# Performance work log

Hardware: AMD Instinct MI355X
Metric: run time of the kernel (lower is better)

The kernel has to match this reference:

```python
import jax, jax.numpy as jnp
import numpy as np

MIN_NORM = 1e-15
C = 1.0  # ball curvature from init kwargs
N, D, O = 16384, 512, 512


def _expmap0(u, c):
    sqrt_c = c ** 0.5
    u_norm = jnp.maximum(jnp.linalg.norm(u, axis=-1, keepdims=True), MIN_NORM)
    return jnp.tanh(sqrt_c * u_norm) * u / (sqrt_c * u_norm)


def setup_inputs() -> dict:
    key = jax.random.key(0)
    k1, k2, k3 = jax.random.split(key, 3)
    # scale inputs so they lie inside the unit Poincare ball (E||x|| ~ 0.45)
    x = jax.random.normal(k1, (N, D), jnp.float32) * 0.02
    point = _expmap0(jax.random.normal(k2, (O, D), jnp.float32) / 4, C)
    tangent = jax.random.normal(k3, (O, D), jnp.float32)
    tangent = tangent / jnp.maximum(jnp.linalg.norm(tangent, axis=-1, keepdims=True), MIN_NORM)  # sphere proj_
    scale = jnp.zeros((O,), jnp.float32)
    return {"x": x, "point": point, "tangent": tangent, "scale": scale}


def reference(x, point, tangent, scale):
    """Mobius dist2plane (signed) * exp(scale).

    Computes the reductions of diff = mobius_add(-p, x) analytically so the
    [N, O, D] broadcast intermediate of the original is never materialized.
    """
    c = C
    sqrt_c = c ** 0.5
    p, a = point, tangent
    p2 = jnp.sum(p * p, -1)                 # [O]  ||p||^2
    x2 = jnp.sum(x * x, -1)                 # [N]  ||x||^2
    xp = x @ p.T                             # [N,O] <x, p>
    xy = -xp                                 # <-p, x>
    # mobius_add(-p, x) = (A*(-p) + B*x) / Dn
    A = 1 + 2 * c * xy + c * x2[:, None]     # [N,O] coeff of -p
    B = 1 - c * p2                           # [O]   coeff of x
    Dn = jnp.maximum(1 + 2 * c * xy + (c * c) * p2[None, :] * x2[:, None], MIN_NORM)  # [N,O]
    pa = jnp.sum(p * a, -1)                  # [O]  <p, a>
    xa = x @ a.T                             # [N,O] <x, a>
    diff_norm2 = (A * A * p2[None, :] - 2 * A * B[None, :] * xp
                  + (B * B)[None, :] * x2[:, None]) / (Dn * Dn)
    diff_norm2 = jnp.maximum(diff_norm2, MIN_NORM)
    sc_diff_a = (-A * pa[None, :] + B[None, :] * xa) / Dn  # <diff, a>
    a_norm = jnp.maximum(jnp.linalg.norm(a, axis=-1), MIN_NORM)  # [O]
    num = 2 * sqrt_c * sc_diff_a
    denom = jnp.maximum((1 - c * diff_norm2) * a_norm[None, :], MIN_NORM)
    dist = jnp.arcsinh(num / denom) / sqrt_c  # [N,O]
    return dist * jnp.exp(scale)
```

## Files before the change

kernel.cpp:

```cpp
#include <hip/hip_runtime.h>
#include <hip/hip_bf16.h>

typedef float f32x4 __attribute__((ext_vector_type(4)));
typedef short short8_t __attribute__((ext_vector_type(8)));

__device__ __forceinline__ unsigned int cvt2(float lo, float hi) {
    unsigned int ul = __builtin_bit_cast(unsigned int, lo);
    unsigned int uh = __builtin_bit_cast(unsigned int, hi);
    ul += 0x7FFFu + ((ul >> 16) & 1u);
    uh += 0x7FFFu + ((uh >> 16) & 1u);
    return (ul >> 16) | (uh & 0xFFFF0000u);
}

__device__ __forceinline__ float sq4(f32x4 v, float acc) {
    acc = fmaf(v[0], v[0], acc); acc = fmaf(v[1], v[1], acc);
    acc = fmaf(v[2], v[2], acc); acc = fmaf(v[3], v[3], acc);
    return acc;
}

__device__ __forceinline__ float dot4(f32x4 a, f32x4 b, float acc) {
    acc = fmaf(a[0], b[0], acc); acc = fmaf(a[1], b[1], acc);
    acc = fmaf(a[2], b[2], acc); acc = fmaf(a[3], b[3], acc);
    return acc;
}

__device__ __forceinline__ short8_t pk8(f32x4 a, f32x4 b) {
    union { short8_t s; unsigned int u[4]; } w;
    w.u[0] = cvt2(a[0], a[1]); w.u[1] = cvt2(a[2], a[3]);
    w.u[2] = cvt2(b[0], b[1]); w.u[3] = cvt2(b[2], b[3]);
    return w.s;
}

__device__ __forceinline__ void gload16(const void* g, void* l) {
    __builtin_amdgcn_global_load_lds(
        (const __attribute__((address_space(1))) unsigned int*)g,
        (__attribute__((address_space(3))) unsigned int*)l, 16, 0, 0);
}

__global__ __launch_bounds__(256)
void prep_kernel(const float* __restrict__ X, const float* __restrict__ P,
                 const float* __restrict__ A, const float* __restrict__ S,
                 short* __restrict__ Xb, short* __restrict__ Pb, short* __restrict__ Ab,
                 float* __restrict__ x2a, float* __restrict__ paa, float* __restrict__ Ba,
                 float* __restrict__ rBana, float* __restrict__ esla, int N, int O)
{
    const int D = 512;
    const int w    = blockIdx.x * 4 + (threadIdx.x >> 6);
    const int lane = threadIdx.x & 63;
    if (w < N) {
        const float* row = X + (size_t)w * D + lane * 8;
        f32x4 u0 = *(const f32x4*)row;
        f32x4 u1 = *(const f32x4*)(row + 4);
        *(short8_t*)(Xb + (size_t)w * D + lane * 8) = pk8(u0, u1);
        float s = sq4(u1, sq4(u0, 0.f));
        #pragma unroll
        for (int m = 1; m < 64; m <<= 1) s += __shfl_xor(s, m, 64);
        if (lane == 0) x2a[w] = s;
    } else if (w < N + O) {
        const int col = w - N;
        const float* prow = P + (size_t)col * D + lane * 8;
        const float* arow = A + (size_t)col * D + lane * 8;
        f32x4 p0 = *(const f32x4*)prow, p1 = *(const f32x4*)(prow + 4);
        f32x4 a0 = *(const f32x4*)arow, a1 = *(const f32x4*)(arow + 4);
        *(short8_t*)(Pb + (size_t)col * D + lane * 8) = pk8(p0, p1);
        *(short8_t*)(Ab + (size_t)col * D + lane * 8) = pk8(a0, a1);
        float sp  = sq4(p1, sq4(p0, 0.f));
        float sa  = sq4(a1, sq4(a0, 0.f));
        float spa = dot4(p1, a1, dot4(p0, a0, 0.f));
        #pragma unroll
        for (int m = 1; m < 64; m <<= 1) {
            sp += __shfl_xor(sp, m, 64);
            sa += __shfl_xor(sa, m, 64);
            spa += __shfl_xor(spa, m, 64);
        }
        if (lane == 0) {
            float B  = 1.f - sp;
            float an = fmaxf(__builtin_amdgcn_sqrtf(sa), 1e-15f);
            paa[col]   = spa;
            Ba[col]    = B;
            rBana[col] = __builtin_amdgcn_rcpf(fmaxf(B * an, 1e-30f));
            esla[col]  = 0.69314718055994531f * expf(S[col]);
        }
    }
}

#define BM2 64
#define BN2 128
#define BK2 64

__global__ __launch_bounds__(256, 4)
void mobius_gemm_kernel(const short* __restrict__ Xb, const short* __restrict__ Pb,
                        const short* __restrict__ Ab,
                        const float* __restrict__ x2a, const float* __restrict__ paa,
                        const float* __restrict__ Ba, const float* __restrict__ rBana,
                        const float* __restrict__ esla,
                        float* __restrict__ out, int N, int O)
{
    const int D = 512;
    __shared__ __align__(16) char smem[(BM2 + 2 * BN2) * BK2 * 2];
    char* xs = smem;
    char* ps = smem + BM2 * BK2 * 2;
    char* as = smem + (BM2 + BN2) * BK2 * 2;

    const int nwg = gridDim.x;
    const int q   = nwg >> 3;
    const int swz = (blockIdx.x & 7) * q + (blockIdx.x >> 3);
    const int ncol = O / BN2;
    const int brow = swz / ncol, bcol = swz % ncol;
    const int n0 = brow * BM2, o0 = bcol * BN2;

    const int tid = threadIdx.x, lane = tid & 63, wid = tid >> 6;
    const int wr = wid >> 1, wc = wid & 1;

    f32x4 accP[2][4], accA[2][4];
    #pragma unroll
    for (int m = 0; m < 2; m++)
        #pragma unroll
        for (int n = 0; n < 4; n++) { accP[m][n] = (f32x4)0.f; accA[m][n] = (f32x4)0.f; }

    const size_t Db = (size_t)D * 2;

    for (int ks = 0; ks < D / BK2; ++ks) {
        const size_t kb = (size_t)ks * (BK2 * 2);
        #pragma unroll
        for (int s = 0; s < 2; ++s) {
            int cl = s * 256 + tid, row = cl >> 3, ch = cl & 7;
            gload16((const char*)Xb + (size_t)(n0 + row) * Db + kb + ((ch ^ (row & 7)) << 4),
                    xs + cl * 16);
        }
        #pragma unroll
        for (int s = 0; s < 4; ++s) {
            int cl = s * 256 + tid, row = cl >> 3, ch = cl & 7;
            size_t go = (size_t)(o0 + row) * Db + kb + ((ch ^ (row & 7)) << 4);
            gload16((const char*)Pb + go, ps + cl * 16);
            gload16((const char*)Ab + go, as + cl * 16);
        }
        __syncthreads();

        #pragma unroll
        for (int kk = 0; kk < 2; ++kk) {
            const int kx = (kk * 64 + ((lane >> 4) << 4)) ^ ((lane & 7) << 4);
            short8_t af[2], bp[4], ba[4];
            #pragma unroll
            for (int m = 0; m < 2; m++) {
                int row = wr * 32 + m * 16 + (lane & 15);
                af[m] = *(const short8_t*)(xs + (row << 7) + kx);
            }
            #pragma unroll
            for (int n = 0; n < 4; n++) {
                int row = wc * 64 + n * 16 + (lane & 15);
                bp[n] = *(const short8_t*)(ps + (row << 7) + kx);
                ba[n] = *(const short8_t*)(as + (row << 7) + kx);
            }
            #pragma unroll
            for (int m = 0; m < 2; m++)
                #pragma unroll
                for (int n = 0; n < 4; n++) {
                    accP[m][n] = __builtin_amdgcn_mfma_f32_16x16x32_bf16(af[m], bp[n], accP[m][n], 0, 0, 0);
                    accA[m][n] = __builtin_amdgcn_mfma_f32_16x16x32_bf16(af[m], ba[n], accA[m][n], 0, 0, 0);
                }
        }
        __syncthreads();
    }

    const int cl_ = lane & 15, g = lane >> 4;
    float pac[4], Bc[4], rB[4], es[4];
    #pragma unroll
    for (int n = 0; n < 4; n++) {
        int col = o0 + wc * 64 + n * 16 + cl_;
        pac[n] = paa[col]; Bc[n] = Ba[col]; rB[n] = rBana[col]; es[n] = esla[col];
    }
    float* ob = (float*)smem;
    #pragma unroll
    for (int m = 0; m < 2; m++) {
        #pragma unroll
        for (int r = 0; r < 4; r++) {
            const int row = wr * 32 + m * 16 + g * 4 + r;
            const float x2  = x2a[n0 + row];
            const float ap1 = 1.f + x2;
            const float zs  = 2.f * __builtin_amdgcn_rcpf(fmaxf(1.f - x2, 1e-30f));
            #pragma unroll
            for (int n = 0; n < 4; n++) {
                float xp = accP[m][n][r];
                float xa = accA[m][n][r];
                float Ac  = ap1 - (xp + xp);
                float num = fmaf(Bc[n], xa, -(Ac * pac[n]));
                float z   = num * zs * rB[n];
                float az  = fabsf(z);
                float wv  = az + __builtin_amdgcn_sqrtf(fmaf(z, z, 1.f));
                float l   = __builtin_amdgcn_logf(wv);
                ob[row * 132 + wc * 64 + n * 16 + cl_] = copysignf(l, z) * es[n];
            }
        }
    }
    __syncthreads();
    #pragma unroll
    for (int s = 0; s < 8; ++s) {
        int row = s * 8 + (tid >> 5), c = (tid & 31) * 4;
        f32x4 v = *(const f32x4*)(ob + row * 132 + c);
        *(f32x4*)(out + (size_t)(n0 + row) * O + o0 + c) = v;
    }
}

#define BM 128
#define BN 128
#define BK 64
#define PAD 8
#define LDT (BK + PAD)

__global__ __launch_bounds__(256, 2)
void mobius_d2p_kernel(const float* __restrict__ X, const float* __restrict__ P,
                       const float* __restrict__ A, const float* __restrict__ S,
                       float* __restrict__ out, int N, int O, int D)
{
    __shared__ short xs[BM][LDT];
    __shared__ short ps[BM][LDT];
    __shared__ short as_[BM][LDT];
    __shared__ float x2p[BM][2];
    __shared__ float p2p[BM][2];
    __shared__ float pap[BM][2];
    __shared__ float a2p[BM][2];

    const int nwg = gridDim.x;
    int swz = blockIdx.x;
    if ((nwg & 7) == 0) {
        int q = nwg >> 3;
        swz = (blockIdx.x & 7) * q + (blockIdx.x >> 3);
    }
    const int ncol = O / BN;
    const int brow = swz / ncol;
    const int bcol = swz % ncol;
    const int n0 = brow * BM;
    const int o0 = bcol * BN;

    const int tid  = threadIdx.x;
    const int lane = tid & 63;
    const int wid  = tid >> 6;
    const int wr   = wid >> 1;
    const int wc   = wid & 1;

    const int srow = tid >> 1;
    const int sseg = (tid & 1) * 32;

    const float* xg = X + (size_t)(n0 + srow) * D + sseg;
    const float* pg = P + (size_t)(o0 + srow) * D + sseg;
    const float* ag = A + (size_t)(o0 + srow) * D + sseg;

    float accx2 = 0.f, accp2 = 0.f, accpa = 0.f, acca2 = 0.f;

    f32x4 accP[4][4], accA[4][4];
    #pragma unroll
    for (int i = 0; i < 4; i++)
        #pragma unroll
        for (int j = 0; j < 4; j++) { accP[i][j] = (f32x4)0.f; accA[i][j] = (f32x4)0.f; }

    const int frow_a = wr * 64 + (lane & 15);
    const int frow_b = wc * 64 + (lane & 15);
    const int fk     = (lane >> 4) * 8;

    const int nk = D / BK;
    for (int ks = 0; ks < nk; ++ks) {
        const float* xr = xg + ks * BK;
        const float* pr = pg + ks * BK;
        const float* ar = ag + ks * BK;

        #pragma unroll
        for (int j = 0; j < 4; j++) {
            f32x4 u0 = *(const f32x4*)(xr + j * 8);
            f32x4 u1 = *(const f32x4*)(xr + j * 8 + 4);
            accx2 = sq4(u0, accx2); accx2 = sq4(u1, accx2);
            *(short8_t*)&xs[srow][sseg + j * 8] = pk8(u0, u1);
        }
        #pragma unroll
        for (int j = 0; j < 4; j++) {
            f32x4 u0 = *(const f32x4*)(pr + j * 8);
            f32x4 u1 = *(const f32x4*)(pr + j * 8 + 4);
            f32x4 v0 = *(const f32x4*)(ar + j * 8);
            f32x4 v1 = *(const f32x4*)(ar + j * 8 + 4);
            accp2 = sq4(u0, accp2); accp2 = sq4(u1, accp2);
            acca2 = sq4(v0, acca2); acca2 = sq4(v1, acca2);
            accpa = dot4(u0, v0, accpa); accpa = dot4(u1, v1, accpa);
            *(short8_t*)&ps[srow][sseg + j * 8] = pk8(u0, u1);
            *(short8_t*)&as_[srow][sseg + j * 8] = pk8(v0, v1);
        }
        __syncthreads();

        #pragma unroll
        for (int kk = 0; kk < 2; ++kk) {
            const int kof = kk * 32 + fk;
            short8_t af[4], bp[4], ba[4];
            #pragma unroll
            for (int m = 0; m < 4; m++) af[m] = *(const short8_t*)&xs[frow_a + m * 16][kof];
            #pragma unroll
            for (int n = 0; n < 4; n++) {
                bp[n] = *(const short8_t*)&ps[frow_b + n * 16][kof];
                ba[n] = *(const short8_t*)&as_[frow_b + n * 16][kof];
            }
            #pragma unroll
            for (int m = 0; m < 4; m++)
                #pragma unroll
                for (int n = 0; n < 4; n++) {
                    accP[m][n] = __builtin_amdgcn_mfma_f32_16x16x32_bf16(af[m], bp[n], accP[m][n], 0, 0, 0);
                    accA[m][n] = __builtin_amdgcn_mfma_f32_16x16x32_bf16(af[m], ba[n], accA[m][n], 0, 0, 0);
                }
        }
        __syncthreads();
    }

    x2p[srow][tid & 1] = accx2;
    p2p[srow][tid & 1] = accp2;
    pap[srow][tid & 1] = accpa;
    a2p[srow][tid & 1] = acca2;
    __syncthreads();

    const int cl = lane & 15;
    const int g  = lane >> 4;

    float pac[4], Bcv[4], rBan[4], esl[4];
    #pragma unroll
    for (int n = 0; n < 4; n++) {
        int col = wc * 64 + n * 16 + cl;
        float p2 = p2p[col][0] + p2p[col][1];
        float pa = pap[col][0] + pap[col][1];
        float a2 = a2p[col][0] + a2p[col][1];
        float B  = 1.f - p2;
        float an = fmaxf(__builtin_amdgcn_sqrtf(a2), 1e-15f);
        pac[n] = pa; Bcv[n] = B;
        rBan[n] = __builtin_amdgcn_rcpf(fmaxf(B * an, 1e-30f));
        esl[n]  = 0.69314718055994531f * expf(S[o0 + col]);
    }
    float x2r[16];
    #pragma unroll
    for (int m = 0; m < 4; m++)
        #pragma unroll
        for (int r = 0; r < 4; r++) {
            int row = wr * 64 + m * 16 + g * 4 + r;
            x2r[m * 4 + r] = x2p[row][0] + x2p[row][1];
        }

    #pragma unroll
    for (int m = 0; m < 4; m++) {
        #pragma unroll
        for (int r = 0; r < 4; r++) {
            const int row = wr * 64 + m * 16 + g * 4 + r;
            const float x2  = x2r[m * 4 + r];
            const float ap1 = 1.f + x2;
            const float zs  = 2.f * __builtin_amdgcn_rcpf(fmaxf(1.f - x2, 1e-30f));
            float* orow = out + (size_t)(n0 + row) * O + o0 + wc * 64 + cl;
            #pragma unroll
            for (int n = 0; n < 4; n++) {
                float xp = accP[m][n][r];
                float xa = accA[m][n][r];
                float Ac = ap1 - (xp + xp);
                float num = fmaf(Bcv[n], xa, -(Ac * pac[n]));
                float z   = num * zs * rBan[n];
                float az = fabsf(z);
                float w  = az + __builtin_amdgcn_sqrtf(fmaf(z, z, 1.f));
                float l  = __builtin_amdgcn_logf(w);
                orow[n * 16] = copysignf(l, z) * esl[n];
            }
        }
    }
}

extern "C" void kernel_launch(void* const* d_in, const int* in_sizes, int n_in,
                              void* d_out, int out_size, void* d_ws, size_t ws_size,
                              hipStream_t stream) {
    const float* X = (const float*)d_in[0];
    const float* P = (const float*)d_in[1];
    const float* A = (const float*)d_in[2];
    const float* S = (const float*)d_in[3];
    float* out = (float*)d_out;

    const int O = in_sizes[3];
    const int D = in_sizes[1] / O;
    const int N = in_sizes[0] / D;

    size_t offP  = (size_t)N * D * 2;
    size_t offA  = offP + (size_t)O * D * 2;
    size_t offx2 = offA + (size_t)O * D * 2;
    size_t offpa = offx2 + (size_t)N * 4;
    size_t offB  = offpa + (size_t)O * 4;
    size_t offrB = offB + (size_t)O * 4;
    size_t offes = offrB + (size_t)O * 4;
    size_t need  = offes + (size_t)O * 4;

    const bool fast = (ws_size >= need) && D == 512 &&
                      (N % BM2 == 0) && (O % BN2 == 0) &&
                      (((N / BM2) * (O / BN2)) % 8 == 0) && ((N + O) % 4 == 0);

    if (fast) {
        char* ws = (char*)d_ws;
        short* Xb = (short*)ws;
        short* Pb = (short*)(ws + offP);
        short* Ab = (short*)(ws + offA);
        float* x2a = (float*)(ws + offx2);
        float* paa = (float*)(ws + offpa);
        float* Ba  = (float*)(ws + offB);
        float* rBa = (float*)(ws + offrB);
        float* esl = (float*)(ws + offes);

        prep_kernel<<<dim3((N + O) / 4), dim3(256), 0, stream>>>(
            X, P, A, S, Xb, Pb, Ab, x2a, paa, Ba, rBa, esl, N, O);
        mobius_gemm_kernel<<<dim3((N / BM2) * (O / BN2)), dim3(256), 0, stream>>>(
            Xb, Pb, Ab, x2a, paa, Ba, rBa, esl, out, N, O);
    } else {
        const int nwg = (N / BM) * (O / BN);
        mobius_d2p_kernel<<<dim3(nwg), dim3(256), 0, stream>>>(X, P, A, S, out, N, O, D);
    }
}
```

Before: 113.9 us.

## Double-buffer LDS tiles with halved K step in Mobius GEMM

The single-buffered K loop becomes a ping-pong scheme over two LDS buffers, with BK reduced from 64 to 32. The next K slice is staged while MFMAs run on the current one, which is meant to hide global-load latency behind compute and to drop one barrier per iteration. The XOR swizzle on LDS tile addresses is removed, so the 64-byte row stride may cause LDS bank conflicts on fragment reads. The loop also runs twice as many iterations, each doing less work per barrier.

```diff
diff --git a/kernel.cpp b/kernel.cpp
--- a/kernel.cpp
+++ b/kernel.cpp
@@ -86,7 +86,26 @@
 
 #define BM2 64
 #define BN2 128
-#define BK2 64
+#define BK2 32
+#define BUFB 20480
+
+__device__ __forceinline__ void stage_tiles(const char* Xb, const char* Pb, const char* Ab,
+                                            char* buf, int n0, int o0, int ks, int tid,
+                                            size_t Db) {
+    const size_t kb = (size_t)ks * (BK2 * 2);
+    {
+        int row = tid >> 2, ch = tid & 3;
+        gload16(Xb + (size_t)(n0 + row) * Db + kb + ch * 16, buf + tid * 16);
+    }
+    #pragma unroll
+    for (int s = 0; s < 2; ++s) {
+        int cl = s * 256 + tid;
+        int row = cl >> 2, ch = cl & 3;
+        size_t go = (size_t)(o0 + row) * Db + kb + ch * 16;
+        gload16(Pb + go, buf + 4096 + cl * 16);
+        gload16(Ab + go, buf + 12288 + cl * 16);
+    }
+}
 
 __global__ __launch_bounds__(256, 4)
 void mobius_gemm_kernel(const short* __restrict__ Xb, const short* __restrict__ Pb,
@@ -97,10 +116,7 @@
                         float* __restrict__ out, int N, int O)
 {
     const int D = 512;
-    __shared__ __align__(16) char smem[(BM2 + 2 * BN2) * BK2 * 2];
-    char* xs = smem;
-    char* ps = smem + BM2 * BK2 * 2;
-    char* as = smem + (BM2 + BN2) * BK2 * 2;
+    __shared__ __align__(16) char smem[2][BUFB];
 
     const int nwg = gridDim.x;
     const int q   = nwg >> 3;
@@ -119,48 +135,45 @@
         for (int n = 0; n < 4; n++) { accP[m][n] = (f32x4)0.f; accA[m][n] = (f32x4)0.f; }
 
     const size_t Db = (size_t)D * 2;
-
-    for (int ks = 0; ks < D / BK2; ++ks) {
-        const size_t kb = (size_t)ks * (BK2 * 2);
-        #pragma unroll
-        for (int s = 0; s < 2; ++s) {
-            int cl = s * 256 + tid, row = cl >> 3, ch = cl & 7;
-            gload16((const char*)Xb + (size_t)(n0 + row) * Db + kb + ((ch ^ (row & 7)) << 4),
-                    xs + cl * 16);
-        }
-        #pragma unroll
-        for (int s = 0; s < 4; ++s) {
-            int cl = s * 256 + tid, row = cl >> 3, ch = cl & 7;
-            size_t go = (size_t)(o0 + row) * Db + kb + ((ch ^ (row & 7)) << 4);
-            gload16((const char*)Pb + go, ps + cl * 16);
-            gload16((const char*)Ab + go, as + cl * 16);
-        }
+    const char* Xc = (const char*)Xb;
+    const char* Pc = (const char*)Pb;
+    const char* Ac = (const char*)Ab;
+
+    const int fr = lane & 15;
+    const int fo = (lane >> 4) << 4;
+
+    stage_tiles(Xc, Pc, Ac, smem[0], n0, o0, 0, tid, Db);
+    __syncthreads();
+
+    int cur = 0;
+    const int NK = D / BK2;
+    for (int ks = 0; ks < NK; ++ks) {
+        if (ks + 1 < NK)
+            stage_tiles(Xc, Pc, Ac, smem[cur ^ 1], n0, o0, ks + 1, tid, Db);
+
+        const char* xs = smem[cur];
+        const char* ps = smem[cur] + 4096;
+        const char* as = smem[cur] + 12288;
+
+        short8_t af[2], bp[4], ba[4];
+        #pragma unroll
+        for (int m = 0; m < 2; m++)
+            af[m] = *(const short8_t*)(xs + (wr * 32 + m * 16 + fr) * 64 + fo);
+        #pragma unroll
+        for (int n = 0; n < 4; n++) {
+            bp[n] = *(const short8_t*)(ps + (wc * 64 + n * 16 + fr) * 64 + fo);
+            ba[n] = *(const short8_t*)(as + (wc * 64 + n * 16 + fr) * 64 + fo);
+        }
+        #pragma unroll
+        for (int m = 0; m < 2; m++)
+            #pragma unroll
+            for (int n = 0; n < 4; n++) {
+                accP[m][n] = __builtin_amdgcn_mfma_f32_16x16x32_bf16(af[m], bp[n], accP[m][n], 0, 0, 0);
+                accA[m][n] = __builtin_amdgcn_mfma_f32_16x16x32_bf16(af[m], ba[n], accA[m][n], 0, 0, 0);
+            }
+
         __syncthreads();
-
-        #pragma unroll
-        for (int kk = 0; kk < 2; ++kk) {
-            const int kx = (kk * 64 + ((lane >> 4) << 4)) ^ ((lane & 7) << 4);
-            short8_t af[2], bp[4], ba[4];
-            #pragma unroll
-            for (int m = 0; m < 2; m++) {
-                int row = wr * 32 + m * 16 + (lane & 15);
-                af[m] = *(const short8_t*)(xs + (row << 7) + kx);
-            }
-            #pragma unroll
-            for (int n = 0; n < 4; n++) {
-                int row = wc * 64 + n * 16 + (lane & 15);
-                bp[n] = *(const short8_t*)(ps + (row << 7) + kx);
-                ba[n] = *(const short8_t*)(as + (row << 7) + kx);
-            }
-            #pragma unroll
-            for (int m = 0; m < 2; m++)
-                #pragma unroll
-                for (int n = 0; n < 4; n++) {
-                    accP[m][n] = __builtin_amdgcn_mfma_f32_16x16x32_bf16(af[m], bp[n], accP[m][n], 0, 0, 0);
-                    accA[m][n] = __builtin_amdgcn_mfma_f32_16x16x32_bf16(af[m], ba[n], accA[m][n], 0, 0, 0);
-                }
-        }
-        __syncthreads();
+        cur ^= 1;
     }
 
     const int cl_ = lane & 15, g = lane >> 4;
@@ -183,8 +196,8 @@
             for (int n = 0; n < 4; n++) {
                 float xp = accP[m][n][r];
                 float xa = accA[m][n][r];
-                float Ac  = ap1 - (xp + xp);
-                float num = fmaf(Bc[n], xa, -(Ac * pac[n]));
+                float Acf = ap1 - (xp + xp);
+                float num = fmaf(Bc[n], xa, -(Acf * pac[n]));
                 float z   = num * zs * rB[n];
                 float az  = fabsf(z);
                 float wv  = az + __builtin_amdgcn_sqrtf(fmaf(z, z, 1.f));
```

Measured after the change: 130.0 us. 1.14x slower.
